# Kernel tuning notes

Hardware: AMD Instinct MI355X
Metric: run time of the kernel (lower is better)

The kernel has to match this reference:

```python
import jax, jax.numpy as jnp
import numpy as np
from jax import lax

B, C_IN, H, W = 128, 3, 256, 256
C_OUT, K = 16, 3


def setup_inputs() -> dict:
    key = jax.random.key(0)
    k1, k2, k3 = jax.random.split(key, 3)
    x = jax.random.normal(k1, (B, C_IN, H, W), dtype=jnp.float32)
    # PyTorch ConvTranspose2d weight layout: (in_channels, out_channels, kH, kW)
    weight = jax.random.normal(k2, (C_IN, C_OUT, K, K), dtype=jnp.float32) * (1.0 / np.sqrt(C_IN * K * K))
    bias = jax.random.normal(k3, (C_OUT, 1, 1), dtype=jnp.float32)
    return {"x": x, "weight": weight, "bias": bias}


def reference(x, weight, bias):
    # conv_transpose2d(stride=1, padding=0) == full correlation with spatially
    # flipped kernel, with in/out channel axes swapped to OIHW.
    k = weight.shape[-1]
    w = jnp.flip(weight, axis=(2, 3)).transpose(1, 0, 2, 3)  # [C_out, C_in, k, k]
    y = lax.conv_general_dilated(
        x, w,
        window_strides=(1, 1),
        padding=[(k - 1, k - 1), (k - 1, k - 1)],
        dimension_numbers=("NCHW", "OIHW", "NCHW"),
    )  # [B, C_out, H+k-1, W+k-1]
    y = jnp.mean(y, axis=(2, 3), keepdims=True)          # [B, C_out, 1, 1]
    y = y + bias[None]                                   # broadcast [C_out,1,1]
    y = jax.nn.logsumexp(y, axis=1, keepdims=True)       # [B, 1, 1, 1]
    y = jnp.sum(y, axis=(2, 3))                          # [B, 1]
    return y * 10.0
```

## Files before the change

### kernel.cpp

```cpp
#include <hip/hip_runtime.h>

#define BATCH   128
#define C_IN    3
#define C_OUT   16
#define HW      65536
#define PLANES  (BATCH * C_IN)
#define BPP     4
#define NBLK    (PLANES * BPP)
#define F4_PER_PLANE 16384
#define F4_PER_BLOCK (F4_PER_PLANE / BPP)
#define THREADS 256

__global__ __launch_bounds__(THREADS) void plane_partials(
        const float* __restrict__ x, float* __restrict__ part) {
    const float4* xp = (const float4*)x + (size_t)blockIdx.x * F4_PER_BLOCK;
    float acc = 0.0f;
#pragma unroll
    for (int i = 0; i < F4_PER_BLOCK / THREADS; ++i) {
        float4 v = xp[i * THREADS + threadIdx.x];
        acc += (v.x + v.y) + (v.z + v.w);
    }
#pragma unroll
    for (int off = 32; off > 0; off >>= 1)
        acc += __shfl_down(acc, off, 64);
    __shared__ float smem[THREADS / 64];
    const int lane = threadIdx.x & 63;
    const int wv   = threadIdx.x >> 6;
    if (lane == 0) smem[wv] = acc;
    __syncthreads();
    if (threadIdx.x == 0)
        part[blockIdx.x] = (smem[0] + smem[1]) + (smem[2] + smem[3]);
}

__global__ __launch_bounds__(BATCH) void finalize(
        const float* __restrict__ part,
        const float* __restrict__ weight,
        const float* __restrict__ bias,
        float* __restrict__ out) {
    __shared__ float Wsum[C_IN][C_OUT];
    __shared__ float bsh[C_OUT];
    const int t = threadIdx.x;
    if (t < C_IN * C_OUT) {
        float s = 0.0f;
#pragma unroll
        for (int k = 0; k < 9; ++k) s += weight[t * 9 + k];
        Wsum[t / C_OUT][t % C_OUT] = s;
    }
    if (t < C_OUT) bsh[t] = bias[t];
    __syncthreads();

    float S[C_IN];
#pragma unroll
    for (int ci = 0; ci < C_IN; ++ci) {
        float s = 0.0f;
#pragma unroll
        for (int k = 0; k < BPP; ++k)
            s += part[(t * C_IN + ci) * BPP + k];
        S[ci] = s;
    }

    const float inv_area = 1.0f / (258.0f * 258.0f);
    float m[C_OUT];
    float mmax = -1e30f;
#pragma unroll
    for (int co = 0; co < C_OUT; ++co) {
        float v = (S[0] * Wsum[0][co] + S[1] * Wsum[1][co] + S[2] * Wsum[2][co])
                      * inv_area + bsh[co];
        m[co] = v;
        mmax = fmaxf(mmax, v);
    }
    float se = 0.0f;
#pragma unroll
    for (int co = 0; co < C_OUT; ++co) se += expf(m[co] - mmax);
    out[t] = 10.0f * (logf(se) + mmax);
}

extern "C" void kernel_launch(void* const* d_in, const int* in_sizes, int n_in,
                              void* d_out, int out_size, void* d_ws, size_t ws_size,
                              hipStream_t stream) {
    const float* x      = (const float*)d_in[0];
    const float* weight = (const float*)d_in[1];
    const float* bias   = (const float*)d_in[2];
    float* out  = (float*)d_out;
    float* part = (float*)d_ws;

    plane_partials<<<NBLK, THREADS, 0, stream>>>(x, part);
    finalize<<<1, BATCH, 0, stream>>>(part, weight, bias, out);
}
```

Baseline: 149.5 us.

## Fuse plane reduction and logsumexp finalize into one per-batch kernel

Result: no change. 150.9 us (+1.0%).

```diff
diff --git a/kernel.cpp b/kernel.cpp
--- a/kernel.cpp
+++ b/kernel.cpp
@@ -4,75 +4,73 @@
 #define C_IN    3
 #define C_OUT   16
 #define HW      65536
-#define PLANES  (BATCH * C_IN)
-#define BPP     4
-#define NBLK    (PLANES * BPP)
 #define F4_PER_PLANE 16384
-#define F4_PER_BLOCK (F4_PER_PLANE / BPP)
-#define THREADS 256
+#define THREADS 1024
+#define NWAVES  (THREADS / 64)
+#define F4_ITERS (F4_PER_PLANE / THREADS)
 
-__global__ __launch_bounds__(THREADS) void plane_partials(
-        const float* __restrict__ x, float* __restrict__ part) {
-    const float4* xp = (const float4*)x + (size_t)blockIdx.x * F4_PER_BLOCK;
-    float acc = 0.0f;
-#pragma unroll
-    for (int i = 0; i < F4_PER_BLOCK / THREADS; ++i) {
-        float4 v = xp[i * THREADS + threadIdx.x];
-        acc += (v.x + v.y) + (v.z + v.w);
-    }
-#pragma unroll
-    for (int off = 32; off > 0; off >>= 1)
-        acc += __shfl_down(acc, off, 64);
-    __shared__ float smem[THREADS / 64];
-    const int lane = threadIdx.x & 63;
-    const int wv   = threadIdx.x >> 6;
-    if (lane == 0) smem[wv] = acc;
-    __syncthreads();
-    if (threadIdx.x == 0)
-        part[blockIdx.x] = (smem[0] + smem[1]) + (smem[2] + smem[3]);
-}
-
-__global__ __launch_bounds__(BATCH) void finalize(
-        const float* __restrict__ part,
+__global__ __launch_bounds__(THREADS) void fused_batch(
+        const float* __restrict__ x,
         const float* __restrict__ weight,
         const float* __restrict__ bias,
         float* __restrict__ out) {
-    __shared__ float Wsum[C_IN][C_OUT];
-    __shared__ float bsh[C_OUT];
+    const int b = blockIdx.x;
     const int t = threadIdx.x;
-    if (t < C_IN * C_OUT) {
-        float s = 0.0f;
+    const float4* xp = (const float4*)x + (size_t)b * (3 * F4_PER_PLANE);
+
+    float a0 = 0.0f, a1 = 0.0f, a2 = 0.0f;
 #pragma unroll
-        for (int k = 0; k < 9; ++k) s += weight[t * 9 + k];
-        Wsum[t / C_OUT][t % C_OUT] = s;
+    for (int i = 0; i < F4_ITERS; ++i) {
+        float4 v0 = xp[0 * F4_PER_PLANE + i * THREADS + t];
+        float4 v1 = xp[1 * F4_PER_PLANE + i * THREADS + t];
+        float4 v2 = xp[2 * F4_PER_PLANE + i * THREADS + t];
+        a0 += (v0.x + v0.y) + (v0.z + v0.w);
+        a1 += (v1.x + v1.y) + (v1.z + v1.w);
+        a2 += (v2.x + v2.y) + (v2.z + v2.w);
     }
-    if (t < C_OUT) bsh[t] = bias[t];
+
+#pragma unroll
+    for (int off = 32; off > 0; off >>= 1) {
+        a0 += __shfl_down(a0, off, 64);
+        a1 += __shfl_down(a1, off, 64);
+        a2 += __shfl_down(a2, off, 64);
+    }
+    __shared__ float smem[NWAVES][3];
+    const int lane = t & 63;
+    const int wv   = t >> 6;
+    if (lane == 0) { smem[wv][0] = a0; smem[wv][1] = a1; smem[wv][2] = a2; }
     __syncthreads();
 
-    float S[C_IN];
+    if (t == 0) {
+        float S[C_IN] = {0.0f, 0.0f, 0.0f};
 #pragma unroll
-    for (int ci = 0; ci < C_IN; ++ci) {
-        float s = 0.0f;
+        for (int w = 0; w < NWAVES; ++w) {
+            S[0] += smem[w][0];
+            S[1] += smem[w][1];
+            S[2] += smem[w][2];
+        }
+        const float inv_area = 1.0f / (258.0f * 258.0f);
+        float m[C_OUT];
+        float mmax = -1e30f;
 #pragma unroll
-        for (int k = 0; k < BPP; ++k)
-            s += part[(t * C_IN + ci) * BPP + k];
-        S[ci] = s;
+        for (int co = 0; co < C_OUT; ++co) {
+            float v = bias[co];
+#pragma unroll
+            for (int ci = 0; ci < C_IN; ++ci) {
+                float ws9 = 0.0f;
+#pragma unroll
+                for (int k = 0; k < 9; ++k)
+                    ws9 += weight[(ci * C_OUT + co) * 9 + k];
+                v += S[ci] * ws9 * inv_area;
+            }
+            m[co] = v;
+            mmax = fmaxf(mmax, v);
+        }
+        float se = 0.0f;
+#pragma unroll
+        for (int co = 0; co < C_OUT; ++co) se += expf(m[co] - mmax);
+        out[b] = 10.0f * (logf(se) + mmax);
     }
-
-    const float inv_area = 1.0f / (258.0f * 258.0f);
-    float m[C_OUT];
-    float mmax = -1e30f;
-#pragma unroll
-    for (int co = 0; co < C_OUT; ++co) {
-        float v = (S[0] * Wsum[0][co] + S[1] * Wsum[1][co] + S[2] * Wsum[2][co])
-                      * inv_area + bsh[co];
-        m[co] = v;
-        mmax = fmaxf(mmax, v);
-    }
-    float se = 0.0f;
-#pragma unroll
-    for (int co = 0; co < C_OUT; ++co) se += expf(m[co] - mmax);
-    out[t] = 10.0f * (logf(se) + mmax);
 }
 
 extern "C" void kernel_launch(void* const* d_in, const int* in_sizes, int n_in,
@@ -81,9 +79,7 @@
     const float* x      = (const float*)d_in[0];
     const float* weight = (const float*)d_in[1];
     const float* bias   = (const float*)d_in[2];
-    float* out  = (float*)d_out;
-    float* part = (float*)d_ws;
+    float* out = (float*)d_out;
 
-    plane_partials<<<NBLK, THREADS, 0, stream>>>(x, part);
-    finalize<<<1, BATCH, 0, stream>>>(part, weight, bias, out);
+    fused_batch<<<BATCH, THREADS, 0, stream>>>(x, weight, bias, out);
 }
```
